# Kernel optimization log

Hardware: AMD Instinct MI355X
Metric: run time of the kernel (lower is better)

## Reference

```python
import jax, jax.numpy as jnp
import numpy as np

NUM_CENTROIDS = 8192
COMMITMENT = 0.25


def setup_inputs() -> dict:
    key = jax.random.key(0)
    k1, k2 = jax.random.split(key)
    B, T, D, K = 16, 2048, 512, NUM_CENTROIDS
    inputs = jax.random.normal(k1, (B, T, D), dtype=jnp.float32)
    # kaiming_normal_ on [K, D]: std = sqrt(2 / fan_in) with fan_in = D
    codebook = jax.random.normal(k2, (K, D), dtype=jnp.float32) * jnp.sqrt(2.0 / D)
    return {"inputs": inputs, "codebook": codebook, "train": 0}


def reference(inputs, codebook, train):
    D = inputs.shape[-1]
    K = codebook.shape[0]
    flat = inputs.reshape(-1, D)  # [N, D]

    distances = (
        jnp.sum(flat * flat, axis=1, keepdims=True)
        - 2.0 * (flat @ codebook.T)
        + jnp.sum(codebook * codebook, axis=1)[None, :]
    )
    nn_idx = jnp.argmin(distances, axis=1)  # [N]

    # one_hot @ codebook == gather (same math, no [N, K] one-hot materialized)
    quantized = codebook[nn_idx]  # [N, D]

    # VQ loss (codebook term) + commitment term
    quant_loss = jnp.square(quantized - jax.lax.stop_gradient(flat))
    quant_loss = quant_loss + COMMITMENT * jnp.square(
        jax.lax.stop_gradient(quantized) - flat
    )
    quantization_loss = quant_loss.reshape(inputs.shape)

    quantized = quantized.reshape(inputs.shape)
    # straight-through estimator
    quantized_out = inputs + jax.lax.stop_gradient(quantized - inputs)

    nn_idx = nn_idx.reshape(inputs.shape[:-1])[None, ...]  # [1, B, T]
    codebook_values = jax.lax.stop_gradient(codebook)[None, ...]  # [1, K, D]
    counts = jnp.ones((K,), dtype=jnp.float32)  # train=False: EMA counter untouched (init ones)

    return quantized_out, quantization_loss, nn_idx, codebook_values, counts
```

## Files before the change

kernel.cpp:

```cpp
#include <hip/hip_runtime.h>

#define NROWS 32768
#define DDIM  512
#define KCENT 8192

#define O_LOSS 16777216
#define O_IDX  33554432
#define O_CBV  33587200
#define O_CNT  37781504

typedef float f32x4 __attribute__((ext_vector_type(4)));
typedef _Float16 f16x8 __attribute__((ext_vector_type(8)));

__global__ __launch_bounds__(256) void vq_cvt_swz8(
    const float* __restrict__ src, char* __restrict__ dst)
{
    const int gid = blockIdx.x * 256 + threadIdx.x;
    const int r = gid >> 6, w = gid & 63, dk = w >> 3, u = w & 7;
    const float4* p = (const float4*)(src + (size_t)r * DDIM + (dk*8 + (u ^ (r & 7))) * 8);
    float4 a = p[0], b = p[1];
    f16x8 h;
    h[0]=(_Float16)a.x; h[1]=(_Float16)a.y; h[2]=(_Float16)a.z; h[3]=(_Float16)a.w;
    h[4]=(_Float16)b.x; h[5]=(_Float16)b.y; h[6]=(_Float16)b.z; h[7]=(_Float16)b.w;
    *(f16x8*)(dst + (size_t)gid * 16) = h;
}

__global__ __launch_bounds__(256) void vq_cnorm_kernel(
    const float* __restrict__ CB, float* __restrict__ cnorm, float* __restrict__ counts)
{
    const int wid  = threadIdx.x >> 6;
    const int lane = threadIdx.x & 63;
    const int cid  = blockIdx.x * 4 + wid;
    const float4* p = (const float4*)(CB + (size_t)cid * DDIM + lane * 8);
    float4 a = p[0], b = p[1];
    double s = (double)a.x*a.x + (double)a.y*a.y + (double)a.z*a.z + (double)a.w*a.w
             + (double)b.x*b.x + (double)b.y*b.y + (double)b.z*b.z + (double)b.w*b.w;
    #pragma unroll
    for (int off = 32; off > 0; off >>= 1) s += __shfl_down(s, off);
    if (lane == 0) { cnorm[cid] = (float)s; counts[cid] = 1.0f; }
}

__device__ __forceinline__ void t2_update(float s, int c,
                                          float& v1, int& i1, float& v2, int& i2)
{
    if (s < v1)      { v2 = v1; i2 = i1; v1 = s; i1 = c; }
    else if (s < v2) { v2 = s;  i2 = c; }
}

__device__ __forceinline__ void t2_merge(float b1, int bi1, float b2, int bi2,
                                         float& a1, int& ai1, float& a2, int& ai2)
{
    if (b1 < a1 || (b1 == a1 && bi1 < ai1)) {
        float o1 = a1; int oi1 = ai1;
        a1 = b1; ai1 = bi1;
        if (b2 < o1 || (b2 == o1 && bi2 < oi1)) { a2 = b2; ai2 = bi2; }
        else                                    { a2 = o1; ai2 = oi1; }
    } else {
        if (b1 < a2 || (b1 == a2 && bi1 < ai2)) { a2 = b1; ai2 = bi1; }
    }
}

__device__ __forceinline__ void gl16(const char* g, const char* l)
{
    __builtin_amdgcn_global_load_lds(
        (const __attribute__((address_space(1))) void*)g,
        (__attribute__((address_space(3))) void*)l, 16, 0, 0);
}

__global__ __launch_bounds__(512, 2) void vq_gemm_kernel(
    const char* __restrict__ Xf, const char* __restrict__ Cf,
    const float* __restrict__ cnorm, int* __restrict__ pmini2)
{
    __shared__ __align__(16) char lds[65536];

    const int rb   = blockIdx.x;
    const int t    = threadIdx.x;
    const int lane = t & 63;
    const int wid  = t >> 6;
    const int rg   = wid & 3;
    const int cg   = wid >> 2;
    const int l15  = lane & 15;
    const int lg   = lane >> 4;

    f16x8 Areg[2][16];
    #pragma unroll
    for (int c = 0; c < 2; ++c) {
        __syncthreads();
        #pragma unroll
        for (int i = 0; i < 8; ++i) {
            const int g = i*512 + t;
            gl16(Xf + ((size_t)(rb*128 + c*64 + (g >> 6)))*1024 + (g & 63)*16,
                 &lds[g*16]);
        }
        __syncthreads();
        if ((rg >> 1) == c) {
            #pragma unroll
            for (int m = 0; m < 2; ++m) {
                const int lr = (rg & 1)*32 + m*16 + l15;
                #pragma unroll
                for (int ks = 0; ks < 16; ++ks) {
                    const int ku = ks*4 + lg;
                    Areg[m][ks] = *(const f16x8*)(
                        &lds[lr*1024 + (ku >> 3)*128 + (((ku & 7) ^ (lr & 7)) * 16)]);
                }
            }
        }
    }
    __syncthreads();

    #define STAGE_B(P, buf) {                                                   \
        const int ctP_ = (P) >> 2, sp_ = (P) & 3;                               \
        _Pragma("unroll")                                                       \
        for (int i = 0; i < 4; ++i) {                                           \
            const int g = i*512 + t;                                            \
            gl16(Cf + ((size_t)(ctP_*128 + (g >> 4)))*1024 + sp_*256 + (g & 15)*16, \
                 &lds[(buf)*32768 + g*16]);                                     \
        } }

    f32x4 acc[2][4];
    float rv1[2][4], rv2[2][4];
    int   ri1[2][4], ri2[2][4];
    #pragma unroll
    for (int m = 0; m < 2; ++m)
        #pragma unroll
        for (int n = 0; n < 4; ++n) {
            f32x4 z = {0.f,0.f,0.f,0.f};
            acc[m][n] = z;
            rv1[m][n] = 3.4e38f; rv2[m][n] = 3.4e38f;
            ri1[m][n] = 0x7fffffff; ri2[m][n] = 0x7fffffff;
        }

    STAGE_B(0, 0);
    asm volatile("s_waitcnt vmcnt(0)\n\ts_barrier" ::: "memory");

    const int rB0 = cg*64 +  0 + l15;
    const int rB1 = cg*64 + 16 + l15;
    const int rB2 = cg*64 + 32 + l15;
    const int rB3 = cg*64 + 48 + l15;

    for (int ct = 0; ct < 64; ++ct) {
        #pragma unroll
        for (int ph = 0; ph < 4; ++ph) {
            const int P = ct*4 + ph;
            if (P + 1 < 256) {
                STAGE_B(P + 1, (P + 1) & 1);
                asm volatile("s_waitcnt vmcnt(4)\n\ts_barrier" ::: "memory");
            } else {
                asm volatile("s_waitcnt vmcnt(0)\n\ts_barrier" ::: "memory");
            }
            const char* bb = &lds[(P & 1)*32768];
            #pragma unroll
            for (int ksl = 0; ksl < 4; ++ksl) {
                const int ks  = ph*4 + ksl;
                const int kuF = ksl*4 + lg;
                const int co  = (kuF >> 3)*128;
                const int sl  = kuF & 7;
                f16x8 B0 = *(const f16x8*)(bb + rB0*256 + co + ((sl ^ (rB0 & 7)) * 16));
                f16x8 B1 = *(const f16x8*)(bb + rB1*256 + co + ((sl ^ (rB1 & 7)) * 16));
                f16x8 B2 = *(const f16x8*)(bb + rB2*256 + co + ((sl ^ (rB2 & 7)) * 16));
                f16x8 B3 = *(const f16x8*)(bb + rB3*256 + co + ((sl ^ (rB3 & 7)) * 16));
                #pragma unroll
                for (int m = 0; m < 2; ++m) {
                    acc[m][0] = __builtin_amdgcn_mfma_f32_16x16x32_f16(Areg[m][ks], B0, acc[m][0], 0, 0, 0);
                    acc[m][1] = __builtin_amdgcn_mfma_f32_16x16x32_f16(Areg[m][ks], B1, acc[m][1], 0, 0, 0);
                    acc[m][2] = __builtin_amdgcn_mfma_f32_16x16x32_f16(Areg[m][ks], B2, acc[m][2], 0, 0, 0);
                    acc[m][3] = __builtin_amdgcn_mfma_f32_16x16x32_f16(Areg[m][ks], B3, acc[m][3], 0, 0, 0);
                }
            }
            asm volatile("s_barrier" ::: "memory");
        }
        const int colb = ct*128 + cg*64;
        #pragma unroll
        for (int n = 0; n < 4; ++n) {
            const int col = colb + n*16 + l15;
            const float cn = cnorm[col];
            #pragma unroll
            for (int m = 0; m < 2; ++m) {
                #pragma unroll
                for (int j = 0; j < 4; ++j) {
                    const float s = fmaf(-2.0f, acc[m][n][j], cn);
                    t2_update(s, col, rv1[m][j], ri1[m][j], rv2[m][j], ri2[m][j]);
                }
                f32x4 z = {0.f,0.f,0.f,0.f};
                acc[m][n] = z;
            }
        }
    }
    #undef STAGE_B

    #pragma unroll
    for (int m = 0; m < 2; ++m)
        #pragma unroll
        for (int j = 0; j < 4; ++j) {
            #pragma unroll
            for (int off = 1; off <= 8; off <<= 1) {
                float b1 = __shfl_xor(rv1[m][j], off);
                float b2 = __shfl_xor(rv2[m][j], off);
                int  bi1 = __shfl_xor(ri1[m][j], off);
                int  bi2 = __shfl_xor(ri2[m][j], off);
                t2_merge(b1, bi1, b2, bi2, rv1[m][j], ri1[m][j], rv2[m][j], ri2[m][j]);
            }
        }

    float4* red = (float4*)&lds[0];
    __syncthreads();
    if (l15 == 0) {
        #pragma unroll
        for (int m = 0; m < 2; ++m)
            #pragma unroll
            for (int j = 0; j < 4; ++j) {
                const int rl = rg*32 + m*16 + lg*4 + j;
                float4 w;
                w.x = rv1[m][j]; w.y = __int_as_float(ri1[m][j]);
                w.z = rv2[m][j]; w.w = __int_as_float(ri2[m][j]);
                red[rl*2 + cg] = w;
            }
    }
    __syncthreads();
    if (t < 128) {
        float4 e0 = red[t*2 + 0], e1 = red[t*2 + 1];
        float v1 = e0.x, v2 = e0.z;
        int   i1 = __float_as_int(e0.y), i2 = __float_as_int(e0.w);
        t2_merge(e1.x, __float_as_int(e1.y), e1.z, __float_as_int(e1.w), v1, i1, v2, i2);
        pmini2[(rb*128 + t)*2 + 0] = i1;
        pmini2[(rb*128 + t)*2 + 1] = i2;
    }
}

__global__ __launch_bounds__(256) void vq_resolve_out(
    const float* __restrict__ X, const float* __restrict__ CB,
    const int* __restrict__ pmini2, float* __restrict__ out)
{
    const int wid  = threadIdx.x >> 6;
    const int lane = threadIdx.x & 63;
    const int row  = blockIdx.x * 4 + wid;
    const int i0 = pmini2[row*2 + 0], i1 = pmini2[row*2 + 1];

    const float4* xp = (const float4*)(X + (size_t)row * DDIM + lane * 8);
    float4 xa = xp[0], xb = xp[1];
    const float4* p0 = (const float4*)(CB + (size_t)i0 * DDIM + lane * 8);
    float4 c0a = p0[0], c0b = p0[1];
    const float4* p1 = (const float4*)(CB + (size_t)i1 * DDIM + lane * 8);
    float4 c1a = p1[0], c1b = p1[1];

    double d0 = 0.0, d1 = 0.0, e;
    e = (double)xa.x - c0a.x; d0 += e*e;  e = (double)xa.y - c0a.y; d0 += e*e;
    e = (double)xa.z - c0a.z; d0 += e*e;  e = (double)xa.w - c0a.w; d0 += e*e;
    e = (double)xb.x - c0b.x; d0 += e*e;  e = (double)xb.y - c0b.y; d0 += e*e;
    e = (double)xb.z - c0b.z; d0 += e*e;  e = (double)xb.w - c0b.w; d0 += e*e;
    e = (double)xa.x - c1a.x; d1 += e*e;  e = (double)xa.y - c1a.y; d1 += e*e;
    e = (double)xa.z - c1a.z; d1 += e*e;  e = (double)xa.w - c1a.w; d1 += e*e;
    e = (double)xb.x - c1b.x; d1 += e*e;  e = (double)xb.y - c1b.y; d1 += e*e;
    e = (double)xb.z - c1b.z; d1 += e*e;  e = (double)xb.w - c1b.w; d1 += e*e;
    #pragma unroll
    for (int off = 1; off < 64; off <<= 1) {
        d0 += __shfl_xor(d0, off);
        d1 += __shfl_xor(d1, off);
    }

    const bool w1 = (d1 < d0) || (d1 == d0 && i1 < i0);
    const int idxw = w1 ? i1 : i0;
    float4 qa, qb;
    qa.x = w1 ? c1a.x : c0a.x;  qa.y = w1 ? c1a.y : c0a.y;
    qa.z = w1 ? c1a.z : c0a.z;  qa.w = w1 ? c1a.w : c0a.w;
    qb.x = w1 ? c1b.x : c0b.x;  qb.y = w1 ? c1b.y : c0b.y;
    qb.z = w1 ? c1b.z : c0b.z;  qb.w = w1 ? c1b.w : c0b.w;

    float4 qoa, loa, qob, lob;
    float d, s;
    d = qa.x - xa.x; qoa.x = xa.x + d; s = d*d; loa.x = s + 0.25f*s;
    d = qa.y - xa.y; qoa.y = xa.y + d; s = d*d; loa.y = s + 0.25f*s;
    d = qa.z - xa.z; qoa.z = xa.z + d; s = d*d; loa.z = s + 0.25f*s;
    d = qa.w - xa.w; qoa.w = xa.w + d; s = d*d; loa.w = s + 0.25f*s;
    d = qb.x - xb.x; qob.x = xb.x + d; s = d*d; lob.x = s + 0.25f*s;
    d = qb.y - xb.y; qob.y = xb.y + d; s = d*d; lob.y = s + 0.25f*s;
    d = qb.z - xb.z; qob.z = xb.z + d; s = d*d; lob.z = s + 0.25f*s;
    d = qb.w - xb.w; qob.w = xb.w + d; s = d*d; lob.w = s + 0.25f*s;

    ((float4*)out)[(size_t)row*128 + lane*2 + 0] = qoa;
    ((float4*)out)[(size_t)row*128 + lane*2 + 1] = qob;
    ((float4*)(out + O_LOSS))[(size_t)row*128 + lane*2 + 0] = loa;
    ((float4*)(out + O_LOSS))[(size_t)row*128 + lane*2 + 1] = lob;
    if (lane == 0) out[O_IDX + row] = (float)idxw;
}

extern "C" void kernel_launch(void* const* d_in, const int* in_sizes, int n_in,
                              void* d_out, int out_size, void* d_ws, size_t ws_size,
                              hipStream_t stream)
{
    const float* X  = (const float*)d_in[0];
    const float* CB = (const float*)d_in[1];
    float* out = (float*)d_out;

    char* XsB  = (char*)out;
    char* CBsB = (char*)(out + O_LOSS);

    float* cnorm  = (float*)d_ws;
    int*   pmini2 = (int*)(cnorm + KCENT);

    vq_cvt_swz8<<<(NROWS*64)/256, 256, 0, stream>>>(X, XsB);
    vq_cvt_swz8<<<(KCENT*64)/256, 256, 0, stream>>>(CB, CBsB);
    vq_cnorm_kernel<<<KCENT/4, 256, 0, stream>>>(CB, cnorm, out + O_CNT);
    vq_gemm_kernel<<<NROWS/128, 512, 0, stream>>>(XsB, CBsB, cnorm, pmini2);
    vq_resolve_out<<<NROWS/4, 256, 0, stream>>>(X, CB, pmini2, out);
    hipMemcpyAsync(out + O_CBV, CB, (size_t)KCENT * DDIM * sizeof(float),
                   hipMemcpyDeviceToDevice, stream);
}
```

Baseline: 942.7 us.

## Retile distance GEMM: 64-row blocks with LDS-resident X and 512-column codebook sweeps

Restructures the distance GEMM so each block handles 64 rows with the X tile kept in LDS, while all 8 waves split a 512-column codebook slice. Each stage loads A and B fragments from LDS and issues 16 MFMAs per wave, with the argmin update done once every 16 k-steps. This frees the register-resident A fragments and enlarges per-wave output tiles. In exchange it doubles LDS use to 128KB, which likely limits occupancy to one block per CU, and doubles total codebook reads since the grid has twice as many blocks.

After: 2.053 ms. 118% more time.

```diff
diff --git a/kernel.cpp b/kernel.cpp
--- a/kernel.cpp
+++ b/kernel.cpp
@@ -67,61 +67,59 @@
         (__attribute__((address_space(3))) void*)l, 16, 0, 0);
 }
 
-__global__ __launch_bounds__(512, 2) void vq_gemm_kernel(
+__global__ __launch_bounds__(512, 2) void vq_sweep_kernel(
     const char* __restrict__ Xf, const char* __restrict__ Cf,
     const float* __restrict__ cnorm, int* __restrict__ pmini2)
 {
-    __shared__ __align__(16) char lds[65536];
+    __shared__ __align__(16) char lds[131072];
 
     const int rb   = blockIdx.x;
     const int t    = threadIdx.x;
     const int lane = t & 63;
-    const int wid  = t >> 6;
-    const int rg   = wid & 3;
-    const int cg   = wid >> 2;
+    const int cg   = t >> 6;
     const int l15  = lane & 15;
     const int lg   = lane >> 4;
 
-    f16x8 Areg[2][16];
-    #pragma unroll
-    for (int c = 0; c < 2; ++c) {
-        __syncthreads();
-        #pragma unroll
-        for (int i = 0; i < 8; ++i) {
-            const int g = i*512 + t;
-            gl16(Xf + ((size_t)(rb*128 + c*64 + (g >> 6)))*1024 + (g & 63)*16,
-                 &lds[g*16]);
-        }
-        __syncthreads();
-        if ((rg >> 1) == c) {
-            #pragma unroll
-            for (int m = 0; m < 2; ++m) {
-                const int lr = (rg & 1)*32 + m*16 + l15;
-                #pragma unroll
-                for (int ks = 0; ks < 16; ++ks) {
-                    const int ku = ks*4 + lg;
-                    Areg[m][ks] = *(const f16x8*)(
-                        &lds[lr*1024 + (ku >> 3)*128 + (((ku & 7) ^ (lr & 7)) * 16)]);
-                }
-            }
-        }
-    }
+    #pragma unroll
+    for (int i = 0; i < 8; ++i) {
+        const int d = i*512 + t;
+        gl16(Xf + (size_t)(rb*64 + (d >> 6))*1024 + (d & 63)*16, &lds[d*16]);
+    }
+
+    #define STAGE_B(P1, buf) {                                                    \
+        const int s1_ = (P1) >> 4, k1_ = (P1) & 15;                               \
+        _Pragma("unroll")                                                         \
+        for (int i = 0; i < 4; ++i) {                                             \
+            const int d_ = i*512 + t;                                             \
+            const int c_ = d_ >> 2;                                               \
+            const int v_ = (d_ & 3) ^ ((c_ >> 1) & 3);                            \
+            const int U_ = k1_*4 + v_;                                            \
+            gl16(Cf + (size_t)(s1_*512 + c_)*1024 + (U_ >> 3)*128                 \
+                    + (((U_ & 7) ^ (c_ & 7)) * 16),                               \
+                 &lds[65536 + (buf)*32768 + d_*16]);                              \
+        } }
+
+    STAGE_B(0, 0);
     __syncthreads();
 
-    #define STAGE_B(P, buf) {                                                   \
-        const int ctP_ = (P) >> 2, sp_ = (P) & 3;                               \
-        _Pragma("unroll")                                                       \
-        for (int i = 0; i < 4; ++i) {                                           \
-            const int g = i*512 + t;                                            \
-            gl16(Cf + ((size_t)(ctP_*128 + (g >> 4)))*1024 + sp_*256 + (g & 15)*16, \
-                 &lds[(buf)*32768 + g*16]);                                     \
-        } }
-
-    f32x4 acc[2][4];
-    float rv1[2][4], rv2[2][4];
-    int   ri1[2][4], ri2[2][4];
-    #pragma unroll
-    for (int m = 0; m < 2; ++m)
+    int aro[4], arx[4], bof[4];
+    #pragma unroll
+    for (int m = 0; m < 4; ++m) {
+        const int r = m*16 + l15;
+        aro[m] = r*1024;
+        arx[m] = r & 7;
+    }
+    #pragma unroll
+    for (int n = 0; n < 4; ++n) {
+        const int c = cg*64 + n*16 + l15;
+        bof[n] = c*64 + ((lg ^ ((c >> 1) & 3)) * 16);
+    }
+
+    f32x4 acc[4][4];
+    float rv1[4][4], rv2[4][4];
+    int   ri1[4][4], ri2[4][4];
+    #pragma unroll
+    for (int m = 0; m < 4; ++m)
         #pragma unroll
         for (int n = 0; n < 4; ++n) {
             f32x4 z = {0.f,0.f,0.f,0.f};
@@ -130,66 +128,66 @@
             ri1[m][n] = 0x7fffffff; ri2[m][n] = 0x7fffffff;
         }
 
-    STAGE_B(0, 0);
-    asm volatile("s_waitcnt vmcnt(0)\n\ts_barrier" ::: "memory");
-
-    const int rB0 = cg*64 +  0 + l15;
-    const int rB1 = cg*64 + 16 + l15;
-    const int rB2 = cg*64 + 32 + l15;
-    const int rB3 = cg*64 + 48 + l15;
-
-    for (int ct = 0; ct < 64; ++ct) {
-        #pragma unroll
-        for (int ph = 0; ph < 4; ++ph) {
-            const int P = ct*4 + ph;
-            if (P + 1 < 256) {
-                STAGE_B(P + 1, (P + 1) & 1);
-                asm volatile("s_waitcnt vmcnt(4)\n\ts_barrier" ::: "memory");
-            } else {
-                asm volatile("s_waitcnt vmcnt(0)\n\ts_barrier" ::: "memory");
-            }
-            const char* bb = &lds[(P & 1)*32768];
+    for (int P = 0; P < 256; ++P) {
+        if (P + 1 < 256) {
+            STAGE_B(P + 1, (P + 1) & 1);
+            asm volatile("s_waitcnt vmcnt(4)\n\ts_barrier" ::: "memory");
+        } else {
+            asm volatile("s_waitcnt vmcnt(0)\n\ts_barrier" ::: "memory");
+        }
+        const int k = P & 15;
+        const char* bb = &lds[65536 + (P & 1)*32768];
+        const int kb  = (k >> 1)*128;
+        const int sub = (k & 1)*4 + lg;
+        f16x8 A0 = *(const f16x8*)(&lds[aro[0] + kb + ((sub ^ arx[0]) * 16)]);
+        f16x8 A1 = *(const f16x8*)(&lds[aro[1] + kb + ((sub ^ arx[1]) * 16)]);
+        f16x8 A2 = *(const f16x8*)(&lds[aro[2] + kb + ((sub ^ arx[2]) * 16)]);
+        f16x8 A3 = *(const f16x8*)(&lds[aro[3] + kb + ((sub ^ arx[3]) * 16)]);
+        f16x8 B0 = *(const f16x8*)(bb + bof[0]);
+        f16x8 B1 = *(const f16x8*)(bb + bof[1]);
+        f16x8 B2 = *(const f16x8*)(bb + bof[2]);
+        f16x8 B3 = *(const f16x8*)(bb + bof[3]);
+        acc[0][0] = __builtin_amdgcn_mfma_f32_16x16x32_f16(A0, B0, acc[0][0], 0, 0, 0);
+        acc[0][1] = __builtin_amdgcn_mfma_f32_16x16x32_f16(A0, B1, acc[0][1], 0, 0, 0);
+        acc[0][2] = __builtin_amdgcn_mfma_f32_16x16x32_f16(A0, B2, acc[0][2], 0, 0, 0);
+        acc[0][3] = __builtin_amdgcn_mfma_f32_16x16x32_f16(A0, B3, acc[0][3], 0, 0, 0);
+        acc[1][0] = __builtin_amdgcn_mfma_f32_16x16x32_f16(A1, B0, acc[1][0], 0, 0, 0);
+        acc[1][1] = __builtin_amdgcn_mfma_f32_16x16x32_f16(A1, B1, acc[1][1], 0, 0, 0);
+        acc[1][2] = __builtin_amdgcn_mfma_f32_16x16x32_f16(A1, B2, acc[1][2], 0, 0, 0);
+        acc[1][3] = __builtin_amdgcn_mfma_f32_16x16x32_f16(A1, B3, acc[1][3], 0, 0, 0);
+        acc[2][0] = __builtin_amdgcn_mfma_f32_16x16x32_f16(A2, B0, acc[2][0], 0, 0, 0);
+        acc[2][1] = __builtin_amdgcn_mfma_f32_16x16x32_f16(A2, B1, acc[2][1], 0, 0, 0);
+        acc[2][2] = __builtin_amdgcn_mfma_f32_16x16x32_f16(A2, B2, acc[2][2], 0, 0, 0);
+        acc[2][3] = __builtin_amdgcn_mfma_f32_16x16x32_f16(A2, B3, acc[2][3], 0, 0, 0);
+        acc[3][0] = __builtin_amdgcn_mfma_f32_16x16x32_f16(A3, B0, acc[3][0], 0, 0, 0);
+        acc[3][1] = __builtin_amdgcn_mfma_f32_16x16x32_f16(A3, B1, acc[3][1], 0, 0, 0);
+        acc[3][2] = __builtin_amdgcn_mfma_f32_16x16x32_f16(A3, B2, acc[3][2], 0, 0, 0);
+        acc[3][3] = __builtin_amdgcn_mfma_f32_16x16x32_f16(A3, B3, acc[3][3], 0, 0, 0);
+        asm volatile("s_barrier" ::: "memory");
+
+        if (k == 15) {
+            const int s = P >> 4;
             #pragma unroll
-            for (int ksl = 0; ksl < 4; ++ksl) {
-                const int ks  = ph*4 + ksl;
-                const int kuF = ksl*4 + lg;
-                const int co  = (kuF >> 3)*128;
-                const int sl  = kuF & 7;
-                f16x8 B0 = *(const f16x8*)(bb + rB0*256 + co + ((sl ^ (rB0 & 7)) * 16));
-                f16x8 B1 = *(const f16x8*)(bb + rB1*256 + co + ((sl ^ (rB1 & 7)) * 16));
-                f16x8 B2 = *(const f16x8*)(bb + rB2*256 + co + ((sl ^ (rB2 & 7)) * 16));
-                f16x8 B3 = *(const f16x8*)(bb + rB3*256 + co + ((sl ^ (rB3 & 7)) * 16));
+            for (int n = 0; n < 4; ++n) {
+                const int col = s*512 + cg*64 + n*16 + l15;
+                const float cn = cnorm[col];
                 #pragma unroll
-                for (int m = 0; m < 2; ++m) {
-                    acc[m][0] = __builtin_amdgcn_mfma_f32_16x16x32_f16(Areg[m][ks], B0, acc[m][0], 0, 0, 0);
-                    acc[m][1] = __builtin_amdgcn_mfma_f32_16x16x32_f16(Areg[m][ks], B1, acc[m][1], 0, 0, 0);
-                    acc[m][2] = __builtin_amdgcn_mfma_f32_16x16x32_f16(Areg[m][ks], B2, acc[m][2], 0, 0, 0);
-                    acc[m][3] = __builtin_amdgcn_mfma_f32_16x16x32_f16(Areg[m][ks], B3, acc[m][3], 0, 0, 0);
+                for (int m = 0; m < 4; ++m) {
+                    #pragma unroll
+                    for (int j = 0; j < 4; ++j) {
+                        const float sv = fmaf(-2.0f, acc[m][n][j], cn);
+                        t2_update(sv, col, rv1[m][j], ri1[m][j], rv2[m][j], ri2[m][j]);
+                    }
+                    f32x4 z = {0.f,0.f,0.f,0.f};
+                    acc[m][n] = z;
                 }
             }
-            asm volatile("s_barrier" ::: "memory");
-        }
-        const int colb = ct*128 + cg*64;
-        #pragma unroll
-        for (int n = 0; n < 4; ++n) {
-            const int col = colb + n*16 + l15;
-            const float cn = cnorm[col];
-            #pragma unroll
-            for (int m = 0; m < 2; ++m) {
-                #pragma unroll
-                for (int j = 0; j < 4; ++j) {
-                    const float s = fmaf(-2.0f, acc[m][n][j], cn);
-                    t2_update(s, col, rv1[m][j], ri1[m][j], rv2[m][j], ri2[m][j]);
-                }
-                f32x4 z = {0.f,0.f,0.f,0.f};
-                acc[m][n] = z;
-            }
         }
     }
     #undef STAGE_B
 
     #pragma unroll
-    for (int m = 0; m < 2; ++m)
+    for (int m = 0; m < 4; ++m)
         #pragma unroll
         for (int j = 0; j < 4; ++j) {
             #pragma unroll
@@ -206,24 +204,28 @@
     __syncthreads();
     if (l15 == 0) {
         #pragma unroll
-        for (int m = 0; m < 2; ++m)
+        for (int m = 0; m < 4; ++m)
             #pragma unroll
             for (int j = 0; j < 4; ++j) {
-                const int rl = rg*32 + m*16 + lg*4 + j;
+                const int rl = m*16 + lg*4 + j;
                 float4 w;
                 w.x = rv1[m][j]; w.y = __int_as_float(ri1[m][j]);
                 w.z = rv2[m][j]; w.w = __int_as_float(ri2[m][j]);
-                red[rl*2 + cg] = w;
+                red[rl*8 + cg] = w;
             }
     }
     __syncthreads();
-    if (t < 128) {
-        float4 e0 = red[t*2 + 0], e1 = red[t*2 + 1];
+    if (t < 64) {
+        float4 e0 = red[t*8 + 0];
         float v1 = e0.x, v2 = e0.z;
         int   i1 = __float_as_int(e0.y), i2 = __float_as_int(e0.w);
-        t2_merge(e1.x, __float_as_int(e1.y), e1.z, __float_as_int(e1.w), v1, i1, v2, i2);
-        pmini2[(rb*128 + t)*2 + 0] = i1;
-        pmini2[(rb*128 + t)*2 + 1] = i2;
+        #pragma unroll
+        for (int w = 1; w < 8; ++w) {
+            float4 e = red[t*8 + w];
+            t2_merge(e.x, __float_as_int(e.y), e.z, __float_as_int(e.w), v1, i1, v2, i2);
+        }
+        pmini2[(rb*64 + t)*2 + 0] = i1;
+        pmini2[(rb*64 + t)*2 + 1] = i2;
     }
 }
 
@@ -301,7 +303,7 @@
     vq_cvt_swz8<<<(NROWS*64)/256, 256, 0, stream>>>(X, XsB);
     vq_cvt_swz8<<<(KCENT*64)/256, 256, 0, stream>>>(CB, CBsB);
     vq_cnorm_kernel<<<KCENT/4, 256, 0, stream>>>(CB, cnorm, out + O_CNT);
-    vq_gemm_kernel<<<NROWS/128, 512, 0, stream>>>(XsB, CBsB, cnorm, pmini2);
+    vq_sweep_kernel<<<NROWS/64, 512, 0, stream>>>(XsB, CBsB, cnorm, pmini2);
     vq_resolve_out<<<NROWS/4, 256, 0, stream>>>(X, CB, pmini2, out);
     hipMemcpyAsync(out + O_CBV, CB, (size_t)KCENT * DDIM * sizeof(float),
                    hipMemcpyDeviceToDevice, stream);
```
